# Kernel optimization log

Hardware: AMD Instinct MI355X
Metric: run time of the kernel (lower is better)

## Reference

```python
import jax, jax.numpy as jnp
import numpy as np

B, CI, HI, WI = 64, 3, 96, 96
G = 8
HG, WG = 16, 16
HIDLIN = 512
SIGMA_BOOST = 2.0
EPS = 1e-7
HID = (HI // 4 // 2) * (WI // 4 // 2) * 128  # 12*12*128 = 18432


def _conv(x, w, b):
    # NCHW conv, 3x3, padding 1 (matches nn.Conv2d(kernel_size=3, padding=1))
    y = jax.lax.conv_general_dilated(x, w, (1, 1), ((1, 1), (1, 1)),
                                     dimension_numbers=('NCHW', 'OIHW', 'NCHW'))
    return y + b[None, :, None, None]


def _maxpool(x, k):
    return jax.lax.reduce_window(x, -jnp.inf, jax.lax.max,
                                 (1, 1, k, k), (1, 1, k, k), 'VALID')


def setup_inputs() -> dict:
    key = jax.random.key(0)
    ks = jax.random.split(key, 22)

    def w(k, shape, fan_in):
        return jax.random.normal(k, shape, jnp.float32) * np.float32(1.0 / np.sqrt(fan_in))

    return {
        'image': jax.random.normal(ks[0], (B, CI, HI, WI), jnp.float32),
        'noise': jax.random.normal(ks[1], (B * G, 2), jnp.float32),
        # conv block 1
        'w1a': w(ks[2], (32, CI, 3, 3), CI * 9), 'b1a': jnp.zeros((32,), jnp.float32),
        'w1b': w(ks[3], (32, 32, 3, 3), 32 * 9), 'b1b': jnp.zeros((32,), jnp.float32),
        # conv block 2
        'w2a': w(ks[4], (64, 32, 3, 3), 32 * 9), 'b2a': jnp.zeros((64,), jnp.float32),
        'w2b': w(ks[5], (64, 64, 3, 3), 64 * 9), 'b2b': jnp.zeros((64,), jnp.float32),
        # conv block 3
        'w3a': w(ks[6], (128, 64, 3, 3), 64 * 9), 'b3a': jnp.zeros((128,), jnp.float32),
        'w3b': w(ks[7], (128, 128, 3, 3), 128 * 9), 'b3b': jnp.zeros((128,), jnp.float32),
        # linear head (weights stored (in, out))
        'wl1': w(ks[8], (HID, HIDLIN), HID), 'bl1': jnp.zeros((HIDLIN,), jnp.float32),
        'wl2': w(ks[9], (HIDLIN, HIDLIN), HIDLIN), 'bl2': jnp.zeros((HIDLIN,), jnp.float32),
        'wl3': w(ks[10], (HIDLIN, G * 3), HIDLIN), 'bl3': jnp.zeros((G * 3,), jnp.float32),
    }


def reference(image, noise, w1a, b1a, w1b, b1b, w2a, b2a, w2b, b2b,
              w3a, b3a, w3b, b3b, wl1, bl1, wl2, bl2, wl3, bl3):
    # --- preprocess CNN ---
    x = jax.nn.relu(_conv(image, w1a, b1a))
    x = jax.nn.relu(_conv(x, w1b, b1b))
    x = _maxpool(x, 4)
    x = jax.nn.relu(_conv(x, w2a, b2a))
    x = jax.nn.relu(_conv(x, w2b, b2b))
    x = _maxpool(x, 2)
    x = jax.nn.relu(_conv(x, w3a, b3a))
    x = jax.nn.relu(_conv(x, w3b, b3b))
    x = x.reshape(B, -1)                      # Flatten (C,H,W order, like torch .view)
    x = jax.nn.relu(x @ wl1 + bl1)
    x = jax.nn.relu(x @ wl2 + bl2)            # Linear(HIDLIN,HIDLIN) then the extra ReLU
    prep = (x @ wl3 + bl3).reshape(B * G, 3)  # (b*g, 3)

    means = prep[:, :2]                        # (b*g, 2) raw means
    sraw = prep[:, 2]
    # sparse.transform_sigmas: softplus(s + SIGMA_BOOST) + eps, scaled per spatial dim
    sig = jax.nn.softplus(sraw + SIGMA_BOOST) + EPS
    sigmas = sig[:, None] * jnp.array([HI - 1, WI - 1], jnp.float32)  # (b*g, 2)

    # Normal(means, sigmas).sample() -> reparameterized but detached (torch .sample())
    sample = jax.lax.stop_gradient(means + sigmas * noise)
    # sparse.transform_means over size (hi-hg, wi-wg): sigmoid * (size-1), then round
    msize = jnp.array([HI - HG - 1, WI - WG - 1], jnp.float32)
    pts = jnp.round(jax.nn.sigmoid(sample) * msize).astype(jnp.int32).reshape(B, G, 2)

    # glimpse extraction: the original's b*g python slicing loop -> vmapped dynamic_slice
    src = jax.lax.stop_gradient(image)  # original slices image.data (no grad)

    def ext_one(img, p):
        return jax.lax.dynamic_slice(img, (jnp.int32(0), p[0], p[1]), (CI, HG, WG))

    result = jax.vmap(lambda img, ps: jax.vmap(lambda p: ext_one(img, p))(ps))(src, pts)
    # result: (B, G, CI, HG, WG)
    return result, means.reshape(B, G, 2), sigmas.reshape(B, G, 2)
```

## Files before the change

### kernel.cpp

```cpp
#include <hip/hip_runtime.h>
#include <math.h>

constexpr int BB  = 64;
constexpr int CIc = 3;
constexpr int HIc = 96, WIc = 96;
constexpr int Gc  = 8, HGc = 16, WGc = 16;
constexpr int HIDc = 18432;
constexpr int HIDLINc = 512;

using short8 = __attribute__((ext_vector_type(8))) short;
using s4     = __attribute__((ext_vector_type(4))) short;
using f32x16 = __attribute__((ext_vector_type(16))) float;

__device__ inline unsigned short bfr(float f) {
    unsigned int u = __float_as_uint(f);
    u = (u + 0x7FFFu + ((u >> 16) & 1u)) >> 16;
    return (unsigned short)u;
}
__device__ inline float ubf(unsigned short s) {
    return __uint_as_float(((unsigned int)s) << 16);
}
__device__ inline void tsplit(float v, unsigned short& H, unsigned short& M,
                              unsigned short& L) {
    unsigned int u = __float_as_uint(v);
    H = (unsigned short)(u >> 16);
    float r1 = v - __uint_as_float(u & 0xFFFF0000u);
    unsigned int u1 = __float_as_uint(r1);
    M = (unsigned short)(u1 >> 16);
    float r2 = r1 - __uint_as_float(u1 & 0xFFFF0000u);
    L = (unsigned short)(__float_as_uint(r2) >> 16);
}

__device__ __attribute__((aligned(16))) unsigned short g_wh[9216];
__device__ __attribute__((aligned(16))) unsigned short g_wm[9216];
__device__ __attribute__((aligned(16))) unsigned short g_wl[9216];

__device__ __attribute__((aligned(16))) unsigned short g_w1ah[1536];
__device__ __attribute__((aligned(16))) unsigned short g_w1am[1536];
__device__ __attribute__((aligned(16))) unsigned short g_w1al[1536];

__device__ __attribute__((aligned(16))) unsigned short g_wph[276480];
__device__ __attribute__((aligned(16))) unsigned short g_wpm[276480];
__device__ __attribute__((aligned(16))) unsigned short g_wpl[276480];

__device__ inline void packN_one(const float* __restrict__ w, int CIN, int ofs,
                                 int idx)
{
    int chsz = 288 * CIN;
    int chunk = idx / chsz;
    int t = idx - chunk * chsz;
    int s = t >> 9;
    int rr = t & 511;
    int g = rr >> 8, oc32 = (rr >> 3) & 31, j = rr & 7;
    int nc16 = CIN / 16;
    int tap = s / nc16, c16 = s % nc16;
    int ci = c16 * 16 + g * 8 + j;
    int oc = chunk * 32 + oc32;
    float v = w[((size_t)oc * CIN + ci) * 9 + tap];
    unsigned short h = bfr(v);
    float r1 = v - ubf(h);
    unsigned short m = bfr(r1);
    g_wph[ofs + idx] = h; g_wpm[ofs + idx] = m; g_wpl[ofs + idx] = bfr(r1 - ubf(m));
}

__global__ void pack_all(const float* __restrict__ w1a, const float* __restrict__ w1b,
                         const float* __restrict__ w2a, const float* __restrict__ w2b,
                         const float* __restrict__ w3a, const float* __restrict__ w3b)
{
    int idx = blockIdx.x * 256 + threadIdx.x;
    if (idx < 9216) {
        int j = idx & 7, oc = (idx >> 3) & 31, g = (idx >> 8) & 1, s = idx >> 9;
        int ci = 16 * (s & 1) + 8 * g + j;
        int tap = s >> 1;
        float v = w1b[(oc * 32 + ci) * 9 + tap];
        unsigned short h = bfr(v);
        float r1 = v - ubf(h);
        unsigned short m = bfr(r1);
        g_wh[idx] = h; g_wm[idx] = m; g_wl[idx] = bfr(r1 - ubf(m));
    } else if (idx < 27648) {
        packN_one(w2a, 32, 0, idx - 9216);
    } else if (idx < 64512) {
        packN_one(w2b, 64, 18432, idx - 27648);
    } else if (idx < 138240) {
        packN_one(w3a, 64, 55296, idx - 64512);
    } else if (idx < 285696) {
        packN_one(w3b, 128, 129024, idx - 138240);
    } else if (idx < 287232) {
        int i2 = idx - 285696;
        int j = i2 & 7, oc = (i2 >> 3) & 31, gg = (i2 >> 8) & 1, s = i2 >> 9;
        int k = s * 16 + gg * 8 + j;
        int tap = k >> 2, ci = k & 3;
        float v = (tap < 9 && ci < 3) ? w1a[((size_t)oc * 3 + ci) * 9 + tap] : 0.0f;
        unsigned short h = bfr(v);
        float r1 = v - ubf(h);
        unsigned short m = bfr(r1);
        g_w1ah[i2] = h; g_w1am[i2] = m; g_w1al[i2] = bfr(r1 - ubf(m));
    }
}

__global__ void img_split(const float* __restrict__ image,
                          unsigned short* __restrict__ Ih,
                          unsigned short* __restrict__ Im,
                          unsigned short* __restrict__ Il)
{
    int idx = blockIdx.x * 256 + threadIdx.x;
    if (idx >= 64 * 100 * 100) return;
    int x = idx % 100;
    int t = idx / 100;
    int y = t % 100;
    int b = t / 100;
    s4 H = {0, 0, 0, 0}, M = {0, 0, 0, 0}, L = {0, 0, 0, 0};
    if (y >= 2 && y < 98 && x >= 2 && x < 98) {
#pragma unroll
        for (int ci = 0; ci < 3; ++ci) {
            float v = image[((size_t)(b * 3 + ci) * 96 + (y - 2)) * 96 + (x - 2)];
            unsigned short hh, mm, ll;
            tsplit(v, hh, mm, ll);
            H[ci] = (short)hh; M[ci] = (short)mm; L[ci] = (short)ll;
        }
    }
    *(s4*)(Ih + (size_t)idx * 4) = H;
    *(s4*)(Im + (size_t)idx * 4) = M;
    *(s4*)(Il + (size_t)idx * 4) = L;
}

__device__ inline void bz_one(unsigned short* __restrict__ Xh,
                              unsigned short* __restrict__ Xm,
                              unsigned short* __restrict__ Xl,
                              int PAD, int C, int idx)
{
    int RING = 4 * PAD - 4;
    int ci = idx % C;
    int cell = (idx / C) % RING;
    int b = idx / (C * RING);
    int y, x;
    if (cell < PAD)          { y = 0;       x = cell; }
    else if (cell < 2 * PAD) { y = PAD - 1; x = cell - PAD; }
    else { int t = cell - 2 * PAD; y = 1 + (t >> 1); x = (t & 1) ? PAD - 1 : 0; }
    size_t a = ((size_t)(b * PAD + y) * PAD + x) * C + ci;
    Xh[a] = 0; Xm[a] = 0; Xl[a] = 0;
}

__global__ void border_all(unsigned short* X2h, unsigned short* X2m, unsigned short* X2l,
                           unsigned short* X3h, unsigned short* X3m, unsigned short* X3l,
                           unsigned short* X4h, unsigned short* X4m, unsigned short* X4l,
                           unsigned short* X5h, unsigned short* X5m, unsigned short* X5l)
{
    int idx = blockIdx.x * 256 + threadIdx.x;
    if (idx < 204800)        bz_one(X2h, X2m, X2l, 26, 32, idx);
    else if (idx < 614400)   bz_one(X3h, X3m, X3l, 26, 64, idx - 204800);
    else if (idx < 827392)   bz_one(X4h, X4m, X4l, 14, 64, idx - 614400);
    else if (idx < 1253376)  bz_one(X5h, X5m, X5l, 14, 128, idx - 827392);
}

__global__ __launch_bounds__(256, 4)
void conv1ab(const unsigned short* __restrict__ Ih,
             const unsigned short* __restrict__ Im,
             const unsigned short* __restrict__ Il,
             const float* __restrict__ b1a, const float* __restrict__ b1b,
             unsigned short* __restrict__ X2h, unsigned short* __restrict__ X2m,
             unsigned short* __restrict__ X2l)
{
    const int id    = blockIdx.x;
    const int xcd   = id & 7;
    const int local = id >> 3;
    const int gblk  = xcd * 576 + local;
    const int b  = gblk / 72;
    const int r  = gblk % 72;
    const int yq = r / 3;
    const int xt = r % 3;

    const int tid = threadIdx.x;
    const int wave = tid >> 6, lane = tid & 63;
    const int col = lane & 31, g = lane >> 5;

    __shared__ __align__(16) short s_hml[3][6][34][20];
    __shared__ float s_pool[4][8][2][16];
    __shared__ float s_b1a[32], s_b1b[32];
    if (tid < 32) { s_b1a[tid] = b1a[tid]; s_b1b[tid] = b1b[tid]; }
    __syncthreads();

    auto convA = [&](int tile, f32x16& acc) {
        int p = tile * 32 + col;
        int pc = p < 204 ? p : 203;
        int lr = pc / 34, lc = pc - (pc / 34) * 34;
        const size_t ibase =
            ((size_t)(b * 100 + 4 * yq + lr) * 100 + 32 * xt + lc) * 4;
#pragma unroll
        for (int s = 0; s < 3; ++s) {
            int tap0 = 4 * s + 2 * g; if (tap0 > 8) tap0 = 8;
            int tap1 = 4 * s + 2 * g + 1; if (tap1 > 8) tap1 = 8;
            int o0 = ((tap0 / 3) * 100 + tap0 % 3) * 4;
            int o1 = ((tap1 / 3) * 100 + tap1 % 3) * 4;
            s4 h0 = *(const s4*)(Ih + ibase + o0);
            s4 h1 = *(const s4*)(Ih + ibase + o1);
            s4 m0 = *(const s4*)(Im + ibase + o0);
            s4 m1 = *(const s4*)(Im + ibase + o1);
            s4 l0 = *(const s4*)(Il + ibase + o0);
            s4 l1 = *(const s4*)(Il + ibase + o1);
            short8 bh = __builtin_shufflevector(h0, h1, 0, 1, 2, 3, 4, 5, 6, 7);
            short8 bm = __builtin_shufflevector(m0, m1, 0, 1, 2, 3, 4, 5, 6, 7);
            short8 bl = __builtin_shufflevector(l0, l1, 0, 1, 2, 3, 4, 5, 6, 7);
            const int aidx = s * 512 + g * 256 + col * 8;
            short8 ah = *(const short8*)(g_w1ah + aidx);
            short8 am = *(const short8*)(g_w1am + aidx);
            short8 al = *(const short8*)(g_w1al + aidx);
            acc = __builtin_amdgcn_mfma_f32_32x32x16_bf16(ah, bh, acc, 0, 0, 0);
            acc = __builtin_amdgcn_mfma_f32_32x32x16_bf16(ah, bm, acc, 0, 0, 0);
            acc = __builtin_amdgcn_mfma_f32_32x32x16_bf16(am, bh, acc, 0, 0, 0);
            acc = __builtin_amdgcn_mfma_f32_32x32x16_bf16(am, bm, acc, 0, 0, 0);
            acc = __builtin_amdgcn_mfma_f32_32x32x16_bf16(al, bh, acc, 0, 0, 0);
            acc = __builtin_amdgcn_mfma_f32_32x32x16_bf16(ah, bl, acc, 0, 0, 0);
        }
    };

    f32x16 accA0 = {0,0,0,0,0,0,0,0,0,0,0,0,0,0,0,0};
    f32x16 accA1 = {0,0,0,0,0,0,0,0,0,0,0,0,0,0,0,0};
    convA(wave * 2, accA0);
    if (wave != 3) convA(wave * 2 + 1, accA1);

    f32x16 acc0 = {0,0,0,0,0,0,0,0,0,0,0,0,0,0,0,0};
    f32x16 acc1 = {0,0,0,0,0,0,0,0,0,0,0,0,0,0,0,0};

#pragma unroll
    for (int half = 0; half < 2; ++half) {
        if (half) __syncthreads();

#pragma unroll
        for (int t = 0; t < 2; ++t) {
            int tile = wave * 2 + t;
            int p = tile * 32 + col;
            if (tile < 7 && p < 204) {
                const f32x16& A = t ? accA1 : accA0;
                int lr = p / 34, lc = p - (p / 34) * 34;
                s4 H0, M0, L0, H1, M1, L1;
#pragma unroll
                for (int i = 0; i < 4; ++i) {
                    float v0 = fmaxf(A[8 * half + i] +
                                     s_b1a[16 * half + 4 * g + i], 0.0f);
                    float v1 = fmaxf(A[8 * half + 4 + i] +
                                     s_b1a[16 * half + 8 + 4 * g + i], 0.0f);
                    unsigned short hh, mm, ll;
                    tsplit(v0, hh, mm, ll);
                    H0[i] = (short)hh; M0[i] = (short)mm; L0[i] = (short)ll;
                    tsplit(v1, hh, mm, ll);
                    H1[i] = (short)hh; M1[i] = (short)mm; L1[i] = (short)ll;
                }
                *(s4*)&s_hml[0][lr][lc][4 * g]     = H0;
                *(s4*)&s_hml[0][lr][lc][8 + 4 * g] = H1;
                *(s4*)&s_hml[1][lr][lc][4 * g]     = M0;
                *(s4*)&s_hml[1][lr][lc][8 + 4 * g] = M1;
                *(s4*)&s_hml[2][lr][lc][4 * g]     = L0;
                *(s4*)&s_hml[2][lr][lc][8 + 4 * g] = L1;
            }
        }
        __syncthreads();

        __builtin_amdgcn_s_setprio(1);
#pragma unroll
        for (int tap = 0; tap < 9; ++tap) {
            const int s = tap * 2 + half;
            const int dy = tap / 3, dx = tap % 3;
            const int aidx = s * 512 + g * 256 + col * 8;

            s4 a0 = *(const s4*)(&s_hml[0][wave + dy][col + dx][g * 8]);
            s4 a1 = *(const s4*)(&s_hml[0][wave + dy][col + dx][g * 8 + 4]);
            s4 b0 = *(const s4*)(&s_hml[1][wave + dy][col + dx][g * 8]);
            s4 b1 = *(const s4*)(&s_hml[1][wave + dy][col + dx][g * 8 + 4]);
            s4 c0 = *(const s4*)(&s_hml[2][wave + dy][col + dx][g * 8]);
            s4 c1 = *(const s4*)(&s_hml[2][wave + dy][col + dx][g * 8 + 4]);

            short8 bh = __builtin_shufflevector(a0, a1, 0, 1, 2, 3, 4, 5, 6, 7);
            short8 bm = __builtin_shufflevector(b0, b1, 0, 1, 2, 3, 4, 5, 6, 7);
            short8 bl = __builtin_shufflevector(c0, c1, 0, 1, 2, 3, 4, 5, 6, 7);

            short8 ah = *(const short8*)(g_wh + aidx);
            short8 am = *(const short8*)(g_wm + aidx);
            short8 al = *(const short8*)(g_wl + aidx);

            acc0 = __builtin_amdgcn_mfma_f32_32x32x16_bf16(ah, bh, acc0, 0, 0, 0);
            acc1 = __builtin_amdgcn_mfma_f32_32x32x16_bf16(ah, bm, acc1, 0, 0, 0);
            acc0 = __builtin_amdgcn_mfma_f32_32x32x16_bf16(am, bh, acc0, 0, 0, 0);
            acc1 = __builtin_amdgcn_mfma_f32_32x32x16_bf16(am, bm, acc1, 0, 0, 0);
            acc0 = __builtin_amdgcn_mfma_f32_32x32x16_bf16(al, bh, acc0, 0, 0, 0);
            acc1 = __builtin_amdgcn_mfma_f32_32x32x16_bf16(ah, bl, acc1, 0, 0, 0);
        }
        __builtin_amdgcn_s_setprio(0);
    }
    __syncthreads();

#pragma unroll
    for (int rr = 0; rr < 16; ++rr) {
        int ocr = (rr & 3) + 8 * (rr >> 2) + 4 * g;
        float v = fmaxf(acc0[rr] + acc1[rr] + s_b1b[ocr], 0.0f);
        v = fmaxf(v, __shfl_xor(v, 1));
        v = fmaxf(v, __shfl_xor(v, 2));
        if ((col & 3) == 0) s_pool[wave][col >> 2][g][rr] = v;
    }
    __syncthreads();

    {
        int oc = tid & 31, pc = tid >> 5;
        if (pc < 8) {
            int gg = (oc >> 2) & 1;
            int rr = (oc & 3) + (((oc >> 3) & 3) << 2);
            float mv = s_pool[0][pc][gg][rr];
            mv = fmaxf(mv, s_pool[1][pc][gg][rr]);
            mv = fmaxf(mv, s_pool[2][pc][gg][rr]);
            mv = fmaxf(mv, s_pool[3][pc][gg][rr]);
            unsigned short h, m, l;
            tsplit(mv, h, m, l);
            size_t oa = ((size_t)(b * 26 + yq + 1) * 26 + xt * 8 + pc + 1) * 32 + oc;
            X2h[oa] = h; X2m[oa] = m; X2l[oa] = l;
        }
    }
}

template<int CIN, int HW, int NCHUNK, int OUTMODE>
__global__ __launch_bounds__(256)
void convN_mfma(const unsigned short* __restrict__ Xh,
                const unsigned short* __restrict__ Xm,
                const unsigned short* __restrict__ Xl,
                int wofs, const float* __restrict__ bias,
                unsigned short* __restrict__ Yh,
                unsigned short* __restrict__ Ym,
                unsigned short* __restrict__ Yl,
                float* __restrict__ Yf)
{
    constexpr int PAD = HW + 2;
    constexpr int NC16 = CIN / 16;
    constexpr int CHSZ = 288 * CIN;
    constexpr int COUT = NCHUNK * 32;

    const int tid = threadIdx.x;
    const int cpx = gridDim.x >> 3;
    const int blk = (blockIdx.x & 7) * cpx + (blockIdx.x >> 3);
    const int wid = blk * 4 + (tid >> 6);
    const int lane = tid & 63;
    const int col = lane & 31, g = lane >> 5;

    const int chunk = wid % NCHUNK;
    const int wt = wid / NCHUNK;
    const int P = wt * 32 + col;
    const int b = P / (HW * HW);
    const int rem = P - b * (HW * HW);
    const int y = rem / HW, x = rem - y * HW;

    const size_t ib = ((size_t)(b * PAD + y) * PAD + x) * CIN + g * 8;
    const int wbase = wofs + chunk * CHSZ;

    f32x16 acc0 = {0,0,0,0,0,0,0,0,0,0,0,0,0,0,0,0};
    f32x16 acc1 = {0,0,0,0,0,0,0,0,0,0,0,0,0,0,0,0};

#pragma unroll
    for (int tap = 0; tap < 9; ++tap) {
        const int dy = tap / 3, dx = tap % 3;
        for (int c16 = 0; c16 < NC16; ++c16) {
            const int s = tap * NC16 + c16;
            const int aidx = wbase + s * 512 + g * 256 + col * 8;
            const size_t xo = ib + (size_t)((dy * PAD + dx) * CIN + c16 * 16);
            short8 ah = *(const short8*)(g_wph + aidx);
            short8 am = *(const short8*)(g_wpm + aidx);
            short8 al = *(const short8*)(g_wpl + aidx);
            short8 bh = *(const short8*)(Xh + xo);
            short8 bm = *(const short8*)(Xm + xo);
            short8 bl = *(const short8*)(Xl + xo);
            acc0 = __builtin_amdgcn_mfma_f32_32x32x16_bf16(ah, bh, acc0, 0, 0, 0);
            acc1 = __builtin_amdgcn_mfma_f32_32x32x16_bf16(ah, bm, acc1, 0, 0, 0);
            acc0 = __builtin_amdgcn_mfma_f32_32x32x16_bf16(am, bh, acc0, 0, 0, 0);
            acc1 = __builtin_amdgcn_mfma_f32_32x32x16_bf16(am, bm, acc1, 0, 0, 0);
            acc0 = __builtin_amdgcn_mfma_f32_32x32x16_bf16(al, bh, acc0, 0, 0, 0);
            acc1 = __builtin_amdgcn_mfma_f32_32x32x16_bf16(ah, bl, acc1, 0, 0, 0);
        }
    }

    if constexpr (OUTMODE == 0) {
        const size_t obase =
            ((size_t)(b * PAD + y + 1) * PAD + (x + 1)) * COUT + chunk * 32;
#pragma unroll
        for (int q = 0; q < 4; ++q) {
            s4 H, M, L;
#pragma unroll
            for (int i = 0; i < 4; ++i) {
                int r = q * 4 + i;
                int ocr = i + 8 * q + 4 * g;
                float v = fmaxf(acc0[r] + acc1[r] + bias[chunk * 32 + ocr], 0.0f);
                unsigned short h, m, l;
                tsplit(v, h, m, l);
                H[i] = (short)h; M[i] = (short)m; L[i] = (short)l;
            }
            *(s4*)(Yh + obase + 8 * q + 4 * g) = H;
            *(s4*)(Ym + obase + 8 * q + 4 * g) = M;
            *(s4*)(Yl + obase + 8 * q + 4 * g) = L;
        }
    } else {
#pragma unroll
        for (int r = 0; r < 16; ++r) {
            int ocr = chunk * 32 + (r & 3) + 8 * (r >> 2) + 4 * g;
            float v = fmaxf(acc0[r] + acc1[r] + bias[ocr], 0.0f);
            Yf[((size_t)(b * COUT + ocr) * HW + y) * HW + x] = v;
        }
    }
}

__global__ __launch_bounds__(256)
void pool2_pack(const float* __restrict__ t2,
                unsigned short* __restrict__ X4h,
                unsigned short* __restrict__ X4m,
                unsigned short* __restrict__ X4l)
{
    int idx = blockIdx.x * 256 + threadIdx.x;
    constexpr int TOT = BB * 144 * 64;
    if (idx >= TOT) return;
    int oc = idx & 63;
    int p = (idx >> 6) % 144;
    int b = idx / (144 * 64);
    int y = p / 12, x = p % 12;
    const float* src = t2 + ((size_t)(b * 64 + oc) * 24 + 2 * y) * 24 + 2 * x;
    float v = fmaxf(fmaxf(src[0], src[1]), fmaxf(src[24], src[25]));
    unsigned short h, m, l;
    tsplit(v, h, m, l);
    size_t oa = ((size_t)(b * 14 + y + 1) * 14 + x + 1) * 64 + oc;
    X4h[oa] = h; X4m[oa] = m; X4l[oa] = l;
}

constexpr int KSPLIT = 64;
__global__ __launch_bounds__(256)
void lin1_partial(const float* __restrict__ x, const float* __restrict__ w,
                  float* __restrict__ partial)
{
    const int j  = threadIdx.x % 64;
    const int bg = threadIdx.x / 64;
    const int jBase = blockIdx.x * 64;
    const int k  = blockIdx.y;
    const int i0 = k * 288;

    __shared__ float s_x[32][68];

    float acc[16];
#pragma unroll
    for (int u = 0; u < 16; ++u) acc[u] = 0.0f;

    for (int ib = 0; ib < 288; ib += 32) {
        __syncthreads();
        {
            int lb = threadIdx.x / 4;
            int lo = (threadIdx.x % 4) * 8;
            const float* src = x + (size_t)lb * HIDc + i0 + ib + lo;
            float4 a0 = *(const float4*)(src);
            float4 a1 = *(const float4*)(src + 4);
            float tmp[8] = {a0.x, a0.y, a0.z, a0.w, a1.x, a1.y, a1.z, a1.w};
#pragma unroll
            for (int r = 0; r < 8; ++r) s_x[lo + r][lb] = tmp[r];
        }
        __syncthreads();

        for (int ii = 0; ii < 32; ++ii) {
            float wv = w[(size_t)(i0 + ib + ii) * HIDLINc + jBase + j];
            const float4* xp = (const float4*)&s_x[ii][bg * 16];
            float4 x0 = xp[0], x1 = xp[1], x2 = xp[2], x3 = xp[3];
            acc[0]  = fmaf(x0.x, wv, acc[0]);
            acc[1]  = fmaf(x0.y, wv, acc[1]);
            acc[2]  = fmaf(x0.z, wv, acc[2]);
            acc[3]  = fmaf(x0.w, wv, acc[3]);
            acc[4]  = fmaf(x1.x, wv, acc[4]);
            acc[5]  = fmaf(x1.y, wv, acc[5]);
            acc[6]  = fmaf(x1.z, wv, acc[6]);
            acc[7]  = fmaf(x1.w, wv, acc[7]);
            acc[8]  = fmaf(x2.x, wv, acc[8]);
            acc[9]  = fmaf(x2.y, wv, acc[9]);
            acc[10] = fmaf(x2.z, wv, acc[10]);
            acc[11] = fmaf(x2.w, wv, acc[11]);
            acc[12] = fmaf(x3.x, wv, acc[12]);
            acc[13] = fmaf(x3.y, wv, acc[13]);
            acc[14] = fmaf(x3.z, wv, acc[14]);
            acc[15] = fmaf(x3.w, wv, acc[15]);
        }
    }

#pragma unroll
    for (int u = 0; u < 16; ++u) {
        int b = bg * 16 + u;
        partial[((size_t)k * 64 + b) * HIDLINc + jBase + j] = acc[u];
    }
}

__global__ void lin1_reduce(const float* __restrict__ partial,
                            const float* __restrict__ bias,
                            float* __restrict__ x1)
{
    int idx = blockIdx.x * blockDim.x + threadIdx.x;
    if (idx >= 64 * HIDLINc) return;
    int j = idx % HIDLINc;
    float s = 0.0f;
    for (int k = 0; k < KSPLIT; ++k)
        s += partial[(size_t)k * 64 * HIDLINc + idx];
    x1[idx] = fmaxf(s + bias[j], 0.0f);
}

__global__ __launch_bounds__(256)
void lin2_k(const float* __restrict__ x1, const float* __restrict__ w,
            const float* __restrict__ bias, float* __restrict__ x2)
{
    const int j  = threadIdx.x % 64;
    const int bl = threadIdx.x / 64;
    const int jBase = blockIdx.x * 64;
    const int b = blockIdx.y * 4 + bl;

    __shared__ float s_x[4][HIDLINc];
    for (int idx = threadIdx.x; idx < 4 * HIDLINc; idx += 256)
        s_x[idx / HIDLINc][idx % HIDLINc] =
            x1[(size_t)(blockIdx.y * 4 + idx / HIDLINc) * HIDLINc + idx % HIDLINc];
    __syncthreads();

    float acc = 0.0f;
    for (int i = 0; i < HIDLINc; ++i)
        acc = fmaf(s_x[bl][i], w[(size_t)i * HIDLINc + jBase + j], acc);
    x2[(size_t)b * HIDLINc + jBase + j] = fmaxf(acc + bias[jBase + j], 0.0f);
}

__global__ void lin3_k(const float* __restrict__ x2, const float* __restrict__ w,
                       const float* __restrict__ bias, float* __restrict__ prep)
{
    int idx = blockIdx.x * blockDim.x + threadIdx.x;
    if (idx >= 64 * 24) return;
    int j = idx % 24, b = idx / 24;
    float acc = bias[j];
    for (int i = 0; i < HIDLINc; ++i)
        acc = fmaf(x2[(size_t)b * HIDLINc + i], w[i * 24 + j], acc);
    prep[idx] = acc;
}

__global__ void head_k(const float* __restrict__ prep, const float* __restrict__ noise,
                       float* __restrict__ outMeans, float* __restrict__ outSigmas,
                       int* __restrict__ pts)
{
    int id = blockIdx.x * blockDim.x + threadIdx.x;
    if (id >= BB * Gc) return;
    float m0 = prep[id * 3 + 0];
    float m1 = prep[id * 3 + 1];
    float sraw = prep[id * 3 + 2];
    float s = sraw + 2.0f;
    float sig = fmaxf(s, 0.0f) + log1pf(expf(-fabsf(s)));
    sig += 1e-7f;
    float sg = sig * 95.0f;
    outMeans[id * 2 + 0] = m0;
    outMeans[id * 2 + 1] = m1;
    outSigmas[id * 2 + 0] = sg;
    outSigmas[id * 2 + 1] = sg;
    float sa0 = m0 + sg * noise[id * 2 + 0];
    float sa1 = m1 + sg * noise[id * 2 + 1];
    float t0 = 1.0f / (1.0f + expf(-sa0));
    float t1 = 1.0f / (1.0f + expf(-sa1));
    pts[id * 2 + 0] = (int)rintf(t0 * 79.0f);
    pts[id * 2 + 1] = (int)rintf(t1 * 79.0f);
}

__global__ __launch_bounds__(256)
void patch_k(const float* __restrict__ image, const int* __restrict__ pts,
             float* __restrict__ outR)
{
    int id = blockIdx.x;
    int b = id / Gc;
    int p0 = pts[id * 2 + 0];
    int p1 = pts[id * 2 + 1];
    for (int idx = threadIdx.x; idx < CIc * HGc * WGc; idx += 256) {
        int c = idx / (HGc * WGc), rem = idx % (HGc * WGc);
        int hh = rem / WGc, ww = rem % WGc;
        outR[(size_t)id * (CIc * HGc * WGc) + idx] =
            image[((size_t)(b * CIc + c) * HIc + p0 + hh) * WIc + p1 + ww];
    }
}

extern "C" void kernel_launch(void* const* d_in, const int* in_sizes, int n_in,
                              void* d_out, int out_size, void* d_ws, size_t ws_size,
                              hipStream_t stream)
{
    const float* image = (const float*)d_in[0];
    const float* noise = (const float*)d_in[1];
    const float* w1a = (const float*)d_in[2];
    const float* b1a = (const float*)d_in[3];
    const float* w1b = (const float*)d_in[4];
    const float* b1b = (const float*)d_in[5];
    const float* w2a = (const float*)d_in[6];
    const float* b2a = (const float*)d_in[7];
    const float* w2b = (const float*)d_in[8];
    const float* b2b = (const float*)d_in[9];
    const float* w3a = (const float*)d_in[10];
    const float* b3a = (const float*)d_in[11];
    const float* w3b = (const float*)d_in[12];
    const float* b3b = (const float*)d_in[13];
    const float* wl1 = (const float*)d_in[14];
    const float* bl1 = (const float*)d_in[15];
    const float* wl2 = (const float*)d_in[16];
    const float* bl2 = (const float*)d_in[17];
    const float* wl3 = (const float*)d_in[18];
    const float* bl3 = (const float*)d_in[19];

    float* out = (float*)d_out;
    float* ws  = (float*)d_ws;

    unsigned short* X2h = (unsigned short*)(ws + 29884416);
    unsigned short* X2m = (unsigned short*)(ws + 30670848);
    unsigned short* X2l = (unsigned short*)(ws + 31457280);
    unsigned short* X3h = (unsigned short*)(ws);
    unsigned short* X3m = (unsigned short*)(ws + 1572864);
    unsigned short* X3l = (unsigned short*)(ws + 3145728);
    float*  t2  = ws + 4718592;
    unsigned short* X4h = (unsigned short*)(ws + 7340032);
    unsigned short* X4m = (unsigned short*)(ws + 7864320);
    unsigned short* X4l = (unsigned short*)(ws + 8388608);
    unsigned short* X5h = (unsigned short*)(ws + 8912896);
    unsigned short* X5m = (unsigned short*)(ws + 11010048);
    unsigned short* X5l = (unsigned short*)(ws + 12058624);
    float*  t5  = ws + 13107200;
    float*  part= ws + 14680064;
    float*  x1  = ws + 16777216;
    float*  x2  = x1 + 32768;
    float*  prep= x2 + 32768;
    int*    pts = (int*)(prep + 2048);
    unsigned short* Ih = (unsigned short*)(ws + 18874368);
    unsigned short* Im = (unsigned short*)(ws + 20447232);
    unsigned short* Il = (unsigned short*)(ws + 22020096);

    pack_all<<<1122, 256, 0, stream>>>(w1a, w1b, w2a, w2b, w3a, w3b);

    img_split<<<2500, 256, 0, stream>>>(image, Ih, Im, Il);

    border_all<<<4896, 256, 0, stream>>>(X2h, X2m, X2l, X3h, X3m, X3l,
                                         X4h, X4m, X4l, X5h, X5m, X5l);

    conv1ab<<<4608, 256, 0, stream>>>(Ih, Im, Il, b1a, b1b, X2h, X2m, X2l);

    convN_mfma<32, 24, 2, 0><<<576, 256, 0, stream>>>(
        X2h, X2m, X2l, 0, b2a, X3h, X3m, X3l, nullptr);
    convN_mfma<64, 24, 2, 1><<<576, 256, 0, stream>>>(
        X3h, X3m, X3l, 18432, b2b, nullptr, nullptr, nullptr, t2);
    pool2_pack<<<2304, 256, 0, stream>>>(t2, X4h, X4m, X4l);
    convN_mfma<64, 12, 4, 0><<<288, 256, 0, stream>>>(
        X4h, X4m, X4l, 55296, b3a, X5h, X5m, X5l, nullptr);
    convN_mfma<128, 12, 4, 1><<<288, 256, 0, stream>>>(
        X5h, X5m, X5l, 129024, b3b, nullptr, nullptr, nullptr, t5);

    lin1_partial<<<dim3(8, KSPLIT), 256, 0, stream>>>(t5, wl1, part);
    lin1_reduce<<<(64 * HIDLINc + 255) / 256, 256, 0, stream>>>(part, bl1, x1);
    lin2_k<<<dim3(8, 16), 256, 0, stream>>>(x1, wl2, bl2, x2);
    lin3_k<<<6, 256, 0, stream>>>(x2, wl3, bl3, prep);
    head_k<<<2, 256, 0, stream>>>(prep, noise,
                                  out + (size_t)BB * Gc * CIc * HGc * WGc,
                                  out + (size_t)BB * Gc * CIc * HGc * WGc + BB * Gc * 2,
                                  pts);
    patch_k<<<BB * Gc, 256, 0, stream>>>(image, pts, out);
}
```

Measured before the change: 358.8 us.

## Merge weight packing, image split and border zeroing into one prep kernel

Fuses the three preprocessing kernels (weight triple-bf16 packing, image split into padded NHWC, border zeroing of activation buffers) into a single launch indexed by ranges, removing two kernel launches and their gaps. It also raises conv1ab's launch-bounds occupancy hint from 4 to 5 waves per SIMD. Separately, it adds two more cross-term MFMAs (mid×low, low×mid) to conv1a for extra accuracy. The extra MFMAs add compute, and the tighter register budget may cause spills.

```diff
diff --git a/kernel.cpp b/kernel.cpp
--- a/kernel.cpp
+++ b/kernel.cpp
@@ -63,9 +63,32 @@
     g_wph[ofs + idx] = h; g_wpm[ofs + idx] = m; g_wpl[ofs + idx] = bfr(r1 - ubf(m));
 }
 
-__global__ void pack_all(const float* __restrict__ w1a, const float* __restrict__ w1b,
+__device__ inline void bz_one(unsigned short* __restrict__ Xh,
+                              unsigned short* __restrict__ Xm,
+                              unsigned short* __restrict__ Xl,
+                              int PAD, int C, int idx)
+{
+    int RING = 4 * PAD - 4;
+    int ci = idx % C;
+    int cell = (idx / C) % RING;
+    int b = idx / (C * RING);
+    int y, x;
+    if (cell < PAD)          { y = 0;       x = cell; }
+    else if (cell < 2 * PAD) { y = PAD - 1; x = cell - PAD; }
+    else { int t = cell - 2 * PAD; y = 1 + (t >> 1); x = (t & 1) ? PAD - 1 : 0; }
+    size_t a = ((size_t)(b * PAD + y) * PAD + x) * C + ci;
+    Xh[a] = 0; Xm[a] = 0; Xl[a] = 0;
+}
+
+__global__ void prep_all(const float* __restrict__ w1a, const float* __restrict__ w1b,
                          const float* __restrict__ w2a, const float* __restrict__ w2b,
-                         const float* __restrict__ w3a, const float* __restrict__ w3b)
+                         const float* __restrict__ w3a, const float* __restrict__ w3b,
+                         const float* __restrict__ image,
+                         unsigned short* Ih, unsigned short* Im, unsigned short* Il,
+                         unsigned short* X2h, unsigned short* X2m, unsigned short* X2l,
+                         unsigned short* X3h, unsigned short* X3m, unsigned short* X3l,
+                         unsigned short* X4h, unsigned short* X4m, unsigned short* X4l,
+                         unsigned short* X5h, unsigned short* X5m, unsigned short* X5l)
 {
     int idx = blockIdx.x * 256 + threadIdx.x;
     if (idx < 9216) {
@@ -95,65 +118,35 @@
         float r1 = v - ubf(h);
         unsigned short m = bfr(r1);
         g_w1ah[i2] = h; g_w1am[i2] = m; g_w1al[i2] = bfr(r1 - ubf(m));
-    }
-}
-
-__global__ void img_split(const float* __restrict__ image,
-                          unsigned short* __restrict__ Ih,
-                          unsigned short* __restrict__ Im,
-                          unsigned short* __restrict__ Il)
-{
-    int idx = blockIdx.x * 256 + threadIdx.x;
-    if (idx >= 64 * 100 * 100) return;
-    int x = idx % 100;
-    int t = idx / 100;
-    int y = t % 100;
-    int b = t / 100;
-    s4 H = {0, 0, 0, 0}, M = {0, 0, 0, 0}, L = {0, 0, 0, 0};
-    if (y >= 2 && y < 98 && x >= 2 && x < 98) {
-#pragma unroll
-        for (int ci = 0; ci < 3; ++ci) {
-            float v = image[((size_t)(b * 3 + ci) * 96 + (y - 2)) * 96 + (x - 2)];
-            unsigned short hh, mm, ll;
-            tsplit(v, hh, mm, ll);
-            H[ci] = (short)hh; M[ci] = (short)mm; L[ci] = (short)ll;
-        }
-    }
-    *(s4*)(Ih + (size_t)idx * 4) = H;
-    *(s4*)(Im + (size_t)idx * 4) = M;
-    *(s4*)(Il + (size_t)idx * 4) = L;
-}
-
-__device__ inline void bz_one(unsigned short* __restrict__ Xh,
-                              unsigned short* __restrict__ Xm,
-                              unsigned short* __restrict__ Xl,
-                              int PAD, int C, int idx)
-{
-    int RING = 4 * PAD - 4;
-    int ci = idx % C;
-    int cell = (idx / C) % RING;
-    int b = idx / (C * RING);
-    int y, x;
-    if (cell < PAD)          { y = 0;       x = cell; }
-    else if (cell < 2 * PAD) { y = PAD - 1; x = cell - PAD; }
-    else { int t = cell - 2 * PAD; y = 1 + (t >> 1); x = (t & 1) ? PAD - 1 : 0; }
-    size_t a = ((size_t)(b * PAD + y) * PAD + x) * C + ci;
-    Xh[a] = 0; Xm[a] = 0; Xl[a] = 0;
-}
-
-__global__ void border_all(unsigned short* X2h, unsigned short* X2m, unsigned short* X2l,
-                           unsigned short* X3h, unsigned short* X3m, unsigned short* X3l,
-                           unsigned short* X4h, unsigned short* X4m, unsigned short* X4l,
-                           unsigned short* X5h, unsigned short* X5m, unsigned short* X5l)
-{
-    int idx = blockIdx.x * 256 + threadIdx.x;
-    if (idx < 204800)        bz_one(X2h, X2m, X2l, 26, 32, idx);
-    else if (idx < 614400)   bz_one(X3h, X3m, X3l, 26, 64, idx - 204800);
-    else if (idx < 827392)   bz_one(X4h, X4m, X4l, 14, 64, idx - 614400);
-    else if (idx < 1253376)  bz_one(X5h, X5m, X5l, 14, 128, idx - 827392);
-}
-
-__global__ __launch_bounds__(256, 4)
+    } else if (idx < 927232) {
+        int c = idx - 287232;
+        int x = c % 100;
+        int t = c / 100;
+        int y = t % 100;
+        int b = t / 100;
+        s4 H = {0, 0, 0, 0}, M = {0, 0, 0, 0}, L = {0, 0, 0, 0};
+        if (y >= 2 && y < 98 && x >= 2 && x < 98) {
+#pragma unroll
+            for (int ci = 0; ci < 3; ++ci) {
+                float v = image[((size_t)(b * 3 + ci) * 96 + (y - 2)) * 96 + (x - 2)];
+                unsigned short hh, mm, ll;
+                tsplit(v, hh, mm, ll);
+                H[ci] = (short)hh; M[ci] = (short)mm; L[ci] = (short)ll;
+            }
+        }
+        *(s4*)(Ih + (size_t)c * 4) = H;
+        *(s4*)(Im + (size_t)c * 4) = M;
+        *(s4*)(Il + (size_t)c * 4) = L;
+    } else {
+        int c = idx - 927232;
+        if (c < 204800)        bz_one(X2h, X2m, X2l, 26, 32, c);
+        else if (c < 614400)   bz_one(X3h, X3m, X3l, 26, 64, c - 204800);
+        else if (c < 827392)   bz_one(X4h, X4m, X4l, 14, 64, c - 614400);
+        else if (c < 1253376)  bz_one(X5h, X5m, X5l, 14, 128, c - 827392);
+    }
+}
+
+__global__ __launch_bounds__(256, 5)
 void conv1ab(const unsigned short* __restrict__ Ih,
              const unsigned short* __restrict__ Im,
              const unsigned short* __restrict__ Il,
@@ -211,6 +204,8 @@
             acc = __builtin_amdgcn_mfma_f32_32x32x16_bf16(am, bm, acc, 0, 0, 0);
             acc = __builtin_amdgcn_mfma_f32_32x32x16_bf16(al, bh, acc, 0, 0, 0);
             acc = __builtin_amdgcn_mfma_f32_32x32x16_bf16(ah, bl, acc, 0, 0, 0);
+            acc = __builtin_amdgcn_mfma_f32_32x32x16_bf16(am, bl, acc, 0, 0, 0);
+            acc = __builtin_amdgcn_mfma_f32_32x32x16_bf16(al, bm, acc, 0, 0, 0);
         }
     };
 
@@ -623,12 +618,10 @@
     unsigned short* Im = (unsigned short*)(ws + 20447232);
     unsigned short* Il = (unsigned short*)(ws + 22020096);
 
-    pack_all<<<1122, 256, 0, stream>>>(w1a, w1b, w2a, w2b, w3a, w3b);
-
-    img_split<<<2500, 256, 0, stream>>>(image, Ih, Im, Il);
-
-    border_all<<<4896, 256, 0, stream>>>(X2h, X2m, X2l, X3h, X3m, X3l,
-                                         X4h, X4m, X4l, X5h, X5m, X5l);
+    prep_all<<<8518, 256, 0, stream>>>(w1a, w1b, w2a, w2b, w3a, w3b, image,
+                                       Ih, Im, Il,
+                                       X2h, X2m, X2l, X3h, X3m, X3l,
+                                       X4h, X4m, X4l, X5h, X5m, X5l);
 
     conv1ab<<<4608, 256, 0, stream>>>(Ih, Im, Il, b1a, b1b, X2h, X2m, X2l);
 
```

Measured after the change: 354.0 us. About the same (-1.3%).
